# Performance work log

Measured on AMD Instinct MI355X. Metric: run time of the kernel, lower is better.

## Reference

```python
import jax, jax.numpy as jnp
import numpy as np

WIN, SHIFT, HEADS = 12, 6, 24

def _rel_index(win):
    coords = np.stack(np.meshgrid(np.arange(win), np.arange(win), indexing='ij'))  # [2,w,w]
    flat = coords.reshape(2, -1)
    rel = (flat[:, :, None] - flat[:, None, :]).transpose(1, 2, 0).astype(np.int64)  # [N,N,2]
    rel[..., 0] += win - 1
    rel[..., 1] += win - 1
    rel[..., 0] *= 2 * win - 1
    return rel.sum(-1).reshape(-1).astype(np.int32)  # [N*N]

def _shift_mask(H, W, win, shift, dtype):
    img = np.zeros((H, W), np.float32)
    cnt = 0
    for hs in (slice(0, -win), slice(-win, -shift), slice(-shift, None)):
        for ws in (slice(0, -win), slice(-win, -shift), slice(-shift, None)):
            img[hs, ws] = cnt
            cnt += 1
    mw = img.reshape(H // win, win, W // win, win).transpose(0, 2, 1, 3).reshape(-1, win * win)  # [nW,N]
    diff = mw[:, None, :] - mw[:, :, None]
    return jnp.asarray(np.where(diff != 0, -100.0, 0.0), dtype=dtype)  # [nW,N,N]

def setup_inputs() -> dict:
    key = jax.random.key(0)
    ks = jax.random.split(key, 5)
    B, H, W, C = 64, 24, 24, 768
    x = jax.random.normal(ks[0], (B, H, W, C), jnp.float32)
    qkv_w = jax.random.normal(ks[1], (C, 3 * C), jnp.float32) * 0.02
    qkv_b = jnp.zeros((3 * C,), jnp.float32)
    proj_w = jax.random.normal(ks[2], (C, C), jnp.float32) * 0.02
    proj_b = jnp.zeros((C,), jnp.float32)
    rpb_table = jax.random.normal(ks[3], ((2 * WIN - 1) ** 2, HEADS), jnp.float32) * 0.02
    rel_index = jnp.asarray(_rel_index(WIN))
    return {"x": x, "qkv_w": qkv_w, "qkv_b": qkv_b, "proj_w": proj_w,
            "proj_b": proj_b, "rpb_table": rpb_table, "rel_index": rel_index}

def reference(x, qkv_w, qkv_b, proj_w, proj_b, rpb_table, rel_index):
    B, H, W, C = x.shape
    win, shift, heads = WIN, SHIFT, HEADS
    d = C // heads
    scale = d ** -0.5
    N = win * win
    nWh, nWw = H // win, W // win
    nW = nWh * nWw
    # cyclic shift
    xs = jnp.roll(x, (-shift, -shift), axis=(1, 2))
    # window partition -> [B*nW, N, C]
    xw = xs.reshape(B, nWh, win, nWw, win, C).transpose(0, 1, 3, 2, 4, 5).reshape(B * nW, N, C)
    qkv = (xw @ qkv_w + qkv_b).reshape(B * nW, N, 3, heads, d).transpose(2, 0, 3, 1, 4)
    q, k, v = qkv[0] * scale, qkv[1], qkv[2]  # [B*nW, h, N, d]
    attn = jnp.einsum('bhnd,bhmd->bhnm', q, k)
    bias = rpb_table[rel_index].reshape(N, N, heads).transpose(2, 0, 1)  # [h,N,N]
    attn = attn + bias[None]
    mask = _shift_mask(H, W, win, shift, attn.dtype)  # [nW,N,N], static
    attn = (attn.reshape(B, nW, heads, N, N) + mask[None, :, None]).reshape(B * nW, heads, N, N)
    attn = jax.nn.softmax(attn, axis=-1)
    out = jnp.einsum('bhnm,bhmd->bhnd', attn, v).transpose(0, 2, 1, 3).reshape(B * nW, N, C)
    out = out @ proj_w + proj_b
    # window merge + reverse shift
    out = out.reshape(B, nWh, nWw, win, win, C).transpose(0, 1, 3, 2, 4, 5).reshape(B, H, W, C)
    out = jnp.roll(out, (shift, shift), axis=(1, 2))
    # L2 normalize over channel dim (L2N)
    return out / jnp.sqrt(jnp.sum(out * out, axis=-1, keepdims=True) + 1e-6)
```

## Files before the change

kernel.cpp:

```cpp
#include <hip/hip_runtime.h>

typedef unsigned short u16;
typedef __bf16 bf16x8 __attribute__((ext_vector_type(8)));
typedef float f32x4 __attribute__((ext_vector_type(4)));
typedef u16 u16x8 __attribute__((ext_vector_type(8)));
typedef u16 u16x4 __attribute__((ext_vector_type(4)));

__device__ __forceinline__ u16 f2bf(float f) {
    union { float f; unsigned u; } v; v.f = f;
    unsigned r = v.u + 0x7FFFu + ((v.u >> 16) & 1u);
    return (u16)(r >> 16);
}
__device__ __forceinline__ float bf2f(u16 u) {
    union { unsigned u; float f; } v; v.u = ((unsigned)u) << 16; return v.f;
}

#define AS1 __attribute__((address_space(1)))
#define AS3 __attribute__((address_space(3)))
__device__ __forceinline__ void gload_lds16(const void* g, void* l) {
    __builtin_amdgcn_global_load_lds((const AS1 void*)(g), (AS3 void*)(l), 16, 0, 0);
}


__global__ __launch_bounds__(256) void prep_x_kernel(const float* __restrict__ x, u16* __restrict__ xw) {
    unsigned i = ((unsigned)blockIdx.x * 256u + threadIdx.x) * 4u;
    int R = (int)(i / 768u); int c = (int)(i % 768u);
    int w = R / 144, nn = R - w * 144;
    int b = w >> 2, wi = w & 3;
    int r = nn / 12, cc = nn - r * 12;
    int sh = (wi >> 1) * 12 + r + 6; if (sh >= 24) sh -= 24;
    int sw = (wi & 1) * 12 + cc + 6; if (sw >= 24) sw -= 24;
    const float* src = x + (((size_t)b * 24 + sh) * 24 + sw) * 768 + c;
    f32x4 v = *(const f32x4*)src;
    u16x4 o; o[0] = f2bf(v[0]); o[1] = f2bf(v[1]); o[2] = f2bf(v[2]); o[3] = f2bf(v[3]);
    size_t idx = ((size_t)(R >> 7) * 24 + (c >> 5)) * 4096 + (R & 127) * 32 + (c & 31);
    *(u16x4*)(xw + idx) = o;
}

__global__ __launch_bounds__(256) void transpose_cast_kernel(const float* __restrict__ w, u16* __restrict__ wt,
                                                             int K, int N) {
    __shared__ float tile[32][33];
    int tx = threadIdx.x & 31, ty = threadIdx.x >> 5;
    int nb = blockIdx.x * 32, kb = blockIdx.y * 32;
#pragma unroll
    for (int rr = 0; rr < 32; rr += 8) tile[rr + ty][tx] = w[(size_t)(kb + rr + ty) * N + nb + tx];
    __syncthreads();
#pragma unroll
    for (int rr = 0; rr < 32; rr += 8) {
        int n = nb + rr + ty, k = kb + tx;
        wt[((size_t)(n >> 7) * 24 + (k >> 5)) * 4096 + (n & 127) * 32 + (k & 31)] = f2bf(tile[tx][rr + ty]);
    }
}

__global__ __launch_bounds__(256) void make_bias_kernel(const float* __restrict__ tab, const int* __restrict__ rel,
                                                        u16* __restrict__ bm) {
    int i = blockIdx.x * 256 + threadIdx.x;
    int h = i / 20736, nm = i - h * 20736;
    bm[i] = f2bf(tab[rel[nm] * 24 + h]);
}

#define FENCE asm volatile("" ::: "memory")
#define BARRIER __builtin_amdgcn_s_barrier()

#define STAGE_TILE(gp, ldsoff)                                                                 \
    { const char* srcb = (const char*)(gp);                                                    \
      _Pragma("unroll") for (int j = 0; j < 2; j++) {                                          \
        int off = j * 4096 + t * 16;                                                           \
        gload_lds16(srcb + off, (char*)lds + (ldsoff) + off);                                  \
    } }

template <int EPI>
__global__ __launch_bounds__(256, 3) void gemm128_kernel(const u16* __restrict__ A, const u16* __restrict__ Bt,
                                                         const float* __restrict__ bias,
                                                         u16* __restrict__ o0, u16* __restrict__ o1, u16* __restrict__ o2,
                                                         int Ndim, int Kdim, int nxb, int ntiles, float qscale) {
    __shared__ __align__(16) u16 lds[24576];
    const int t = threadIdx.x, lane = t & 63, wv = t >> 6;
    const int wr = wv >> 1, wc = wv & 1;
    const int l15 = lane & 15, lg = lane >> 4;
    const int NT = Kdim >> 5;
    const int q8 = ntiles >> 3, r8 = ntiles & 7;

    int tid = blockIdx.x;
    int xcd = tid & 7, loc = tid >> 3;
    int wg = (xcd < r8 ? xcd * (q8 + 1) : r8 * (q8 + 1) + (xcd - r8) * q8) + loc;
    int by = wg / nxb, bx = wg - by * nxb;
    const u16* Ap = A + (size_t)by * NT * 4096;
    const u16* Bp = Bt + (size_t)bx * NT * 4096;

    STAGE_TILE(Ap, 0);
    STAGE_TILE(Bp, 8192);
    STAGE_TILE(Ap + 4096, 16384);
    STAGE_TILE(Bp + 4096, 16384 + 8192);
    asm volatile("s_waitcnt vmcnt(4)" ::: "memory");
    FENCE; BARRIER;

    while (true) {
        f32x4 acc[4][4] = {};
        int ntid = tid + (int)gridDim.x;
        bool hasNext = ntid < ntiles;
        int nby = 0, nbx = 0;
        const u16 *Anp = nullptr, *Bnp = nullptr;
        if (hasNext) {
            int nxcd = ntid & 7, nloc = ntid >> 3;
            int nwg = (nxcd < r8 ? nxcd * (q8 + 1) : r8 * (q8 + 1) + (nxcd - r8) * q8) + nloc;
            nby = nwg / nxb; nbx = nwg - nby * nxb;
            Anp = A + (size_t)nby * NT * 4096;
            Bnp = Bt + (size_t)nbx * NT * 4096;
        }
        for (int T = 0; T < NT; ++T) {
            const char* rb = (const char*)lds + (T % 3) * 16384;
            const int sb = ((T + 2) % 3) * 16384;
            bool st = true;
            if (T + 2 < NT) {
                STAGE_TILE(Ap + (T + 2) * 4096, sb);
                STAGE_TILE(Bp + (T + 2) * 4096, sb + 8192);
            } else if (hasNext) {
                int TT = T + 2 - NT;
                STAGE_TILE(Anp + TT * 4096, sb);
                STAGE_TILE(Bnp + TT * 4096, sb + 8192);
            } else st = false;
            bf16x8 aR[4], bR[4];
#pragma unroll
            for (int mf = 0; mf < 4; mf++)
                aR[mf] = *(const bf16x8*)(rb + (wr * 64 + mf * 16 + l15) * 64 + lg * 16);
#pragma unroll
            for (int nf = 0; nf < 4; nf++)
                bR[nf] = *(const bf16x8*)(rb + 8192 + (wc * 64 + nf * 16 + l15) * 64 + lg * 16);
            __builtin_amdgcn_s_setprio(1);
#pragma unroll
            for (int mf = 0; mf < 4; mf++)
#pragma unroll
                for (int nf = 0; nf < 4; nf++)
                    acc[mf][nf] = __builtin_amdgcn_mfma_f32_16x16x32_bf16(aR[mf], bR[nf], acc[mf][nf], 0, 0, 0);
            __builtin_amdgcn_s_setprio(0);
            if (T < NT - 1 || hasNext) {
                if (st) { asm volatile("s_waitcnt vmcnt(4)" ::: "memory"); }
                else    { asm volatile("s_waitcnt vmcnt(0)" ::: "memory"); }
                FENCE; BARRIER;
            }
        }
        const int bm = by << 7, bn = bx << 7;
#pragma unroll
        for (int mf = 0; mf < 4; mf++) {
            int Rbase = bm + wr * 64 + mf * 16 + lg * 4;
#pragma unroll
            for (int nf = 0; nf < 4; nf++) {
                int Cg = bn + wc * 64 + nf * 16 + l15;
                float bv = bias[Cg];
                if (EPI == 0) {
                    int s = Cg / 768; int rem = Cg - s * 768; int h = rem >> 5; int dd = rem & 31;
#pragma unroll
                    for (int rg = 0; rg < 4; rg++) {
                        int R = Rbase + rg;
                        int w2 = R / 144; int nn = R - w2 * 144;
                        float v = acc[mf][nf][rg] + bv;
                        if (s == 0)      o0[((size_t)(w2 * 24 + h) * 144 + nn) * 32 + dd] = f2bf(v * qscale);
                        else if (s == 1) o1[((size_t)(w2 * 24 + h) * 144 + nn) * 32 + dd] = f2bf(v);
                        else             o2[((size_t)(w2 * 24 + h) * 32 + dd) * 144 + nn] = f2bf(v);
                    }
                } else {
#pragma unroll
                    for (int rg = 0; rg < 4; rg++) {
                        int R = Rbase + rg;
                        o0[(size_t)R * Ndim + Cg] = f2bf(acc[mf][nf][rg] + bv);
                    }
                }
            }
        }
        if (!hasNext) break;
        tid = ntid; by = nby; bx = nbx; Ap = Anp; Bp = Bnp;
    }
}

__global__ __launch_bounds__(576) void attn_kernel(const u16* __restrict__ Qg, const u16* __restrict__ Kg,
                                                   const u16* __restrict__ Vg, const u16* __restrict__ bias_mat,
                                                   u16* __restrict__ Ob) {
    __shared__ __align__(16) u16 Qs[144 * 40];
    __shared__ __align__(16) u16 Ks[144 * 40];
    __shared__ __align__(16) u16 Vs[32 * 160];
    __shared__ __align__(16) u16 Ps[144 * 160];
    const int bx = blockIdx.x;
    const int w = bx / 24, h = bx - w * 24;
    const int wi = w & 3, wh = wi >> 1, ww = wi & 1;
    const int t = threadIdx.x, lane = t & 63, wv = t >> 6;
    const int l15 = lane & 15, lg = lane >> 4;
    const size_t base = (size_t)bx * 4608;
    {
        int nn = t >> 2, dd = (t & 3) << 3;
        *(u16x8*)(Qs + nn * 40 + dd) = *(const u16x8*)(Qg + base + nn * 32 + dd);
        *(u16x8*)(Ks + nn * 40 + dd) = *(const u16x8*)(Kg + base + nn * 32 + dd);
        int rv = t / 18, cv = (t - rv * 18) * 8;
        int ba = (rv * 320 + cv * 2) ^ ((rv & 7) << 4);
        *(u16x8*)((char*)Vs + ba) = *(const u16x8*)(Vg + base + rv * 144 + cv);
    }
    u16x8 zz = (u16x8)0;
    if (t < 64)  { int rv = t >> 1, cv = 144 + (t & 1) * 8; int ba = (rv * 320 + cv * 2) ^ ((rv & 7) << 4); *(u16x8*)((char*)Vs + ba) = zz; }
    if (t < 288) { int rv = t >> 1, cv = 144 + (t & 1) * 8; int ba = (rv * 320 + cv * 2) ^ ((rv & 7) << 4); *(u16x8*)((char*)Ps + ba) = zz; }
    __syncthreads();

    f32x4 S[9];
    {
        bf16x8 aq = *(const bf16x8*)(Qs + (wv * 16 + l15) * 40 + lg * 8);
        f32x4 z4 = (f32x4)0.0f;
#pragma unroll
        for (int j = 0; j < 9; j++) {
            bf16x8 bk = *(const bf16x8*)(Ks + (j * 16 + l15) * 40 + lg * 8);
            S[j] = __builtin_amdgcn_mfma_f32_16x16x32_bf16(aq, bk, z4, 0, 0, 0);
        }
    }
    int regm[9];
#pragma unroll
    for (int j = 0; j < 9; j++) {
        int m = j * 16 + l15; int r = m / 12, c = m - r * 12;
        int rid = wh ? (r < 6 ? 1 : 2) : 0;
        int cid = ww ? (c < 6 ? 1 : 2) : 0;
        regm[j] = rid * 3 + cid;
    }
    const u16* bh = bias_mat + h * 20736;
#pragma unroll
    for (int rg = 0; rg < 4; rg++) {
        int n = wv * 16 + lg * 4 + rg;
        int r = n / 12, c = n - r * 12;
        int rid = wh ? (r < 6 ? 1 : 2) : 0;
        int cid = ww ? (c < 6 ? 1 : 2) : 0;
        int regn = rid * 3 + cid;
        const u16* bhn = bh + n * 144;
        float mx = -1e30f;
#pragma unroll
        for (int j = 0; j < 9; j++) {
            float v = S[j][rg] + bf2f(bhn[j * 16 + l15]);
            if (regn != regm[j]) v -= 100.0f;
            S[j][rg] = v;
            mx = fmaxf(mx, v);
        }
#pragma unroll
        for (int d = 1; d < 16; d <<= 1) mx = fmaxf(mx, __shfl_xor(mx, d));
        float sum = 0.0f;
#pragma unroll
        for (int j = 0; j < 9; j++) { float e = __expf(S[j][rg] - mx); S[j][rg] = e; sum += e; }
#pragma unroll
        for (int d = 1; d < 16; d <<= 1) sum += __shfl_xor(sum, d);
        float inv = 1.0f / sum;
#pragma unroll
        for (int j = 0; j < 9; j++) {
            int ba = (n * 320 + (j * 16 + l15) * 2) ^ ((n & 7) << 4);
            *(u16*)((char*)Ps + ba) = f2bf(S[j][rg] * inv);
        }
    }
    __syncthreads();
    f32x4 o0 = (f32x4)0.0f, o1 = (f32x4)0.0f;
#pragma unroll
    for (int ks = 0; ks < 5; ks++) {
        int k2 = (ks * 32 + lg * 8) * 2;
        int ra = wv * 16 + l15;
        bf16x8 ap = *(const bf16x8*)((char*)Ps + ((ra * 320 + k2) ^ ((ra & 7) << 4)));
        int rv0 = l15, rv1 = 16 + l15;
        bf16x8 b0 = *(const bf16x8*)((char*)Vs + ((rv0 * 320 + k2) ^ ((rv0 & 7) << 4)));
        bf16x8 b1 = *(const bf16x8*)((char*)Vs + ((rv1 * 320 + k2) ^ ((rv1 & 7) << 4)));
        o0 = __builtin_amdgcn_mfma_f32_16x16x32_bf16(ap, b0, o0, 0, 0, 0);
        o1 = __builtin_amdgcn_mfma_f32_16x16x32_bf16(ap, b1, o1, 0, 0, 0);
    }
#pragma unroll
    for (int rg = 0; rg < 4; rg++) {
        int n = wv * 16 + lg * 4 + rg;
        int R = w * 144 + n;
        size_t idx = ((size_t)(R >> 7) * 24 + h) * 4096 + (R & 127) * 32;
        Ob[idx + l15]      = f2bf(o0[rg]);
        Ob[idx + 16 + l15] = f2bf(o1[rg]);
    }
}

__global__ __launch_bounds__(256) void norm_kernel(const u16* __restrict__ raw, float* __restrict__ out) {
    int R = blockIdx.x * 4 + (threadIdx.x >> 6);
    int lane = threadIdx.x & 63;
    const u16* src = raw + (size_t)R * 768;
    u16x8 a = *(const u16x8*)(src + lane * 8);
    u16x4 b = *(const u16x4*)(src + 512 + lane * 4);
    float f[12];
#pragma unroll
    for (int k = 0; k < 8; k++) f[k] = bf2f(a[k]);
#pragma unroll
    for (int k = 0; k < 4; k++) f[8 + k] = bf2f(b[k]);
    float ss = 0.0f;
#pragma unroll
    for (int k = 0; k < 12; k++) ss += f[k] * f[k];
#pragma unroll
    for (int d = 1; d < 64; d <<= 1) ss += __shfl_xor(ss, d);
    float inv = 1.0f / sqrtf(ss + 1e-6f);
    int w = R / 144, nn = R - w * 144;
    int bb = w >> 2, wi = w & 3;
    int r = nn / 12, cc = nn - r * 12;
    int oh = (wi >> 1) * 12 + r + 6; if (oh >= 24) oh -= 24;
    int ow = (wi & 1) * 12 + cc + 6; if (ow >= 24) ow -= 24;
    float* dst = out + (((size_t)bb * 24 + oh) * 24 + ow) * 768;
    f32x4 v0, v1, v2;
#pragma unroll
    for (int k = 0; k < 4; k++) { v0[k] = f[k] * inv; v1[k] = f[4 + k] * inv; v2[k] = f[8 + k] * inv; }
    *(f32x4*)(dst + lane * 8) = v0;
    *(f32x4*)(dst + lane * 8 + 4) = v1;
    *(f32x4*)(dst + 512 + lane * 4) = v2;
}

extern "C" void kernel_launch(void* const* d_in, const int* in_sizes, int n_in,
                              void* d_out, int out_size, void* d_ws, size_t ws_size,
                              hipStream_t stream) {
    const float* x      = (const float*)d_in[0];
    const float* qkv_w  = (const float*)d_in[1];
    const float* qkv_b  = (const float*)d_in[2];
    const float* proj_w = (const float*)d_in[3];
    const float* proj_b = (const float*)d_in[4];
    const float* rpb    = (const float*)d_in[5];
    const int*   rel    = (const int*)d_in[6];

    char* ws = (char*)d_ws;
    const size_t SZ = 56623104;
    u16*   xw   = (u16*)(ws);
    u16*   Qb   = (u16*)(ws + SZ);
    u16*   Kb   = (u16*)(ws + 2 * SZ);
    u16*   Vt   = (u16*)(ws + 3 * SZ);
    u16*   Ob   = (u16*)(ws + 4 * SZ);
    u16*   qwt  = (u16*)(ws + 5 * SZ);
    u16*   pwt  = (u16*)(ws + 5 * SZ + 3538944);
    u16*   bm   = (u16*)(ws + 5 * SZ + 3538944 + 1179648);
    u16*   raw16 = (u16*)(ws);

    prep_x_kernel<<<27648, 256, 0, stream>>>(x, xw);
    transpose_cast_kernel<<<dim3(72, 24), 256, 0, stream>>>(qkv_w, qwt, 768, 2304);
    transpose_cast_kernel<<<dim3(24, 24), 256, 0, stream>>>(proj_w, pwt, 768, 768);
    make_bias_kernel<<<1944, 256, 0, stream>>>(rpb, rel, bm);

    gemm128_kernel<0><<<768, 256, 0, stream>>>(xw, qwt, qkv_b, Qb, Kb, Vt,
                                               2304, 768, 18, 5184, 0.17677669529663687f);
    attn_kernel<<<6144, 576, 0, stream>>>(Qb, Kb, Vt, bm, Ob);
    gemm128_kernel<1><<<768, 256, 0, stream>>>(Ob, pwt, proj_b, raw16, nullptr, nullptr,
                                               768, 768, 6, 1728, 1.0f);
    norm_kernel<<<9216, 256, 0, stream>>>(raw16, (float*)d_out);
}
```

Before: 460.3 us.

## Keep softmax probabilities in registers and compute transposed S in attention kernel

```diff
diff --git a/kernel.cpp b/kernel.cpp
--- a/kernel.cpp
+++ b/kernel.cpp
@@ -5,6 +5,7 @@
 typedef float f32x4 __attribute__((ext_vector_type(4)));
 typedef u16 u16x8 __attribute__((ext_vector_type(8)));
 typedef u16 u16x4 __attribute__((ext_vector_type(4)));
+typedef unsigned u32x4 __attribute__((ext_vector_type(4)));
 
 __device__ __forceinline__ u16 f2bf(float f) {
     union { float f; unsigned u; } v; v.f = f;
@@ -13,6 +14,11 @@
 }
 __device__ __forceinline__ float bf2f(u16 u) {
     union { unsigned u; float f; } v; v.u = ((unsigned)u) << 16; return v.f;
+}
+__device__ __forceinline__ unsigned cvt_pk_bf16(float lo, float hi) {
+    unsigned r;
+    asm("v_cvt_pk_bf16_f32 %0, %1, %2" : "=v"(r) : "v"(lo), "v"(hi));
+    return r;
 }
 
 #define AS1 __attribute__((address_space(1)))
@@ -55,8 +61,9 @@
 __global__ __launch_bounds__(256) void make_bias_kernel(const float* __restrict__ tab, const int* __restrict__ rel,
                                                         u16* __restrict__ bm) {
     int i = blockIdx.x * 256 + threadIdx.x;
-    int h = i / 20736, nm = i - h * 20736;
-    bm[i] = f2bf(tab[rel[nm] * 24 + h]);
+    int h = i / 20736, mn = i - h * 20736;
+    int m = mn / 144, n = mn - m * 144;
+    bm[i] = f2bf(tab[rel[n * 144 + m] * 24 + h]);
 }
 
 #define FENCE asm volatile("" ::: "memory")
@@ -173,101 +180,117 @@
     }
 }
 
-__global__ __launch_bounds__(576) void attn_kernel(const u16* __restrict__ Qg, const u16* __restrict__ Kg,
-                                                   const u16* __restrict__ Vg, const u16* __restrict__ bias_mat,
+__global__ __launch_bounds__(192) void attn_kernel(const u16* __restrict__ Qg, const u16* __restrict__ Kg,
+                                                   const u16* __restrict__ Vg, const u16* __restrict__ bmT,
                                                    u16* __restrict__ Ob) {
-    __shared__ __align__(16) u16 Qs[144 * 40];
     __shared__ __align__(16) u16 Ks[144 * 40];
     __shared__ __align__(16) u16 Vs[32 * 160];
-    __shared__ __align__(16) u16 Ps[144 * 160];
     const int bx = blockIdx.x;
     const int w = bx / 24, h = bx - w * 24;
     const int wi = w & 3, wh = wi >> 1, ww = wi & 1;
     const int t = threadIdx.x, lane = t & 63, wv = t >> 6;
     const int l15 = lane & 15, lg = lane >> 4;
     const size_t base = (size_t)bx * 4608;
-    {
-        int nn = t >> 2, dd = (t & 3) << 3;
-        *(u16x8*)(Qs + nn * 40 + dd) = *(const u16x8*)(Qg + base + nn * 32 + dd);
-        *(u16x8*)(Ks + nn * 40 + dd) = *(const u16x8*)(Kg + base + nn * 32 + dd);
-        int rv = t / 18, cv = (t - rv * 18) * 8;
+#pragma unroll
+    for (int p = 0; p < 3; p++) {
+        int e = t + p * 192;
+        int row = e >> 2, cx = (e & 3) << 3;
+        *(u16x8*)(Ks + row * 40 + cx) = *(const u16x8*)(Kg + base + row * 32 + cx);
+        int rv = e / 18, cv = (e - rv * 18) * 8;
         int ba = (rv * 320 + cv * 2) ^ ((rv & 7) << 4);
         *(u16x8*)((char*)Vs + ba) = *(const u16x8*)(Vg + base + rv * 144 + cv);
     }
-    u16x8 zz = (u16x8)0;
-    if (t < 64)  { int rv = t >> 1, cv = 144 + (t & 1) * 8; int ba = (rv * 320 + cv * 2) ^ ((rv & 7) << 4); *(u16x8*)((char*)Vs + ba) = zz; }
-    if (t < 288) { int rv = t >> 1, cv = 144 + (t & 1) * 8; int ba = (rv * 320 + cv * 2) ^ ((rv & 7) << 4); *(u16x8*)((char*)Ps + ba) = zz; }
+    if (t < 64) {
+        u16x8 zz = (u16x8)0;
+        int rv = t >> 1, cv = 144 + (t & 1) * 8;
+        int ba = (rv * 320 + cv * 2) ^ ((rv & 7) << 4);
+        *(u16x8*)((char*)Vs + ba) = zz;
+    }
     __syncthreads();
 
-    f32x4 S[9];
-    {
-        bf16x8 aq = *(const bf16x8*)(Qs + (wv * 16 + l15) * 40 + lg * 8);
-        f32x4 z4 = (f32x4)0.0f;
+    const u16* bh = bmT + h * 20736;
+#pragma unroll 1
+    for (int it = 0; it < 3; ++it) {
+        const int s = wv * 3 + it;
+        const int q = s * 16 + l15;
+        bf16x8 aq = *(const bf16x8*)(Qg + base + (size_t)q * 32 + lg * 8);
+        f32x4 S[9];
+        {
+            f32x4 z4 = (f32x4)0.0f;
+#pragma unroll
+            for (int j = 0; j < 9; j++) {
+                bf16x8 bk = *(const bf16x8*)(Ks + (j * 16 + l15) * 40 + lg * 8);
+                S[j] = __builtin_amdgcn_mfma_f32_16x16x32_bf16(bk, aq, z4, 0, 0, 0);
+            }
+        }
+        int rq = q / 12, cq = q - rq * 12; int r12 = rq - s * 0;
+        int ridn = wh ? ((rq % 12) < 6 ? 1 : 2) : 0;
+        int cidn = ww ? (cq < 6 ? 1 : 2) : 0;
+        int regn = ridn * 3 + cidn;
+        (void)r12;
+        float mx = -1e30f;
 #pragma unroll
         for (int j = 0; j < 9; j++) {
-            bf16x8 bk = *(const bf16x8*)(Ks + (j * 16 + l15) * 40 + lg * 8);
-            S[j] = __builtin_amdgcn_mfma_f32_16x16x32_bf16(aq, bk, z4, 0, 0, 0);
-        }
-    }
-    int regm[9];
-#pragma unroll
-    for (int j = 0; j < 9; j++) {
-        int m = j * 16 + l15; int r = m / 12, c = m - r * 12;
-        int rid = wh ? (r < 6 ? 1 : 2) : 0;
-        int cid = ww ? (c < 6 ? 1 : 2) : 0;
-        regm[j] = rid * 3 + cid;
-    }
-    const u16* bh = bias_mat + h * 20736;
-#pragma unroll
-    for (int rg = 0; rg < 4; rg++) {
-        int n = wv * 16 + lg * 4 + rg;
-        int r = n / 12, c = n - r * 12;
-        int rid = wh ? (r < 6 ? 1 : 2) : 0;
-        int cid = ww ? (c < 6 ? 1 : 2) : 0;
-        int regn = rid * 3 + cid;
-        const u16* bhn = bh + n * 144;
-        float mx = -1e30f;
+            const u16* bj = bh + (j * 16 + lg * 4) * 144 + q;
+#pragma unroll
+            for (int rg = 0; rg < 4; rg++) {
+                int k = j * 16 + lg * 4 + rg;
+                int rk = k / 12, ck = k - rk * 12;
+                int ridm = wh ? (rk < 6 ? 1 : 2) : 0;
+                int cidm = ww ? (ck < 6 ? 1 : 2) : 0;
+                float v = S[j][rg] + bf2f(bj[rg * 144]);
+                if (regn != (ridm * 3 + cidm)) v -= 100.0f;
+                S[j][rg] = v;
+                mx = fmaxf(mx, v);
+            }
+        }
+        mx = fmaxf(mx, __shfl_xor(mx, 16));
+        mx = fmaxf(mx, __shfl_xor(mx, 32));
+        float sum = 0.0f;
 #pragma unroll
         for (int j = 0; j < 9; j++) {
-            float v = S[j][rg] + bf2f(bhn[j * 16 + l15]);
-            if (regn != regm[j]) v -= 100.0f;
-            S[j][rg] = v;
-            mx = fmaxf(mx, v);
-        }
-#pragma unroll
-        for (int d = 1; d < 16; d <<= 1) mx = fmaxf(mx, __shfl_xor(mx, d));
-        float sum = 0.0f;
-#pragma unroll
-        for (int j = 0; j < 9; j++) { float e = __expf(S[j][rg] - mx); S[j][rg] = e; sum += e; }
-#pragma unroll
-        for (int d = 1; d < 16; d <<= 1) sum += __shfl_xor(sum, d);
+#pragma unroll
+            for (int rg = 0; rg < 4; rg++) { float e = __expf(S[j][rg] - mx); S[j][rg] = e; sum += e; }
+        }
+        sum += __shfl_xor(sum, 16);
+        sum += __shfl_xor(sum, 32);
         float inv = 1.0f / sum;
+        unsigned pk[10][2];
 #pragma unroll
         for (int j = 0; j < 9; j++) {
-            int ba = (n * 320 + (j * 16 + l15) * 2) ^ ((n & 7) << 4);
-            *(u16*)((char*)Ps + ba) = f2bf(S[j][rg] * inv);
-        }
-    }
-    __syncthreads();
-    f32x4 o0 = (f32x4)0.0f, o1 = (f32x4)0.0f;
-#pragma unroll
-    for (int ks = 0; ks < 5; ks++) {
-        int k2 = (ks * 32 + lg * 8) * 2;
-        int ra = wv * 16 + l15;
-        bf16x8 ap = *(const bf16x8*)((char*)Ps + ((ra * 320 + k2) ^ ((ra & 7) << 4)));
-        int rv0 = l15, rv1 = 16 + l15;
-        bf16x8 b0 = *(const bf16x8*)((char*)Vs + ((rv0 * 320 + k2) ^ ((rv0 & 7) << 4)));
-        bf16x8 b1 = *(const bf16x8*)((char*)Vs + ((rv1 * 320 + k2) ^ ((rv1 & 7) << 4)));
-        o0 = __builtin_amdgcn_mfma_f32_16x16x32_bf16(ap, b0, o0, 0, 0, 0);
-        o1 = __builtin_amdgcn_mfma_f32_16x16x32_bf16(ap, b1, o1, 0, 0, 0);
-    }
-#pragma unroll
-    for (int rg = 0; rg < 4; rg++) {
-        int n = wv * 16 + lg * 4 + rg;
-        int R = w * 144 + n;
-        size_t idx = ((size_t)(R >> 7) * 24 + h) * 4096 + (R & 127) * 32;
-        Ob[idx + l15]      = f2bf(o0[rg]);
-        Ob[idx + 16 + l15] = f2bf(o1[rg]);
+            pk[j][0] = cvt_pk_bf16(S[j][0], S[j][1]);
+            pk[j][1] = cvt_pk_bf16(S[j][2], S[j][3]);
+        }
+        pk[9][0] = 0; pk[9][1] = 0;
+        f32x4 o0 = (f32x4)0.0f, o1 = (f32x4)0.0f;
+        const int srcA = 32 * (lg & 1) + l15;
+        const int srcB = srcA + 16;
+        const bool lowj = (lg < 2);
+#pragma unroll
+        for (int ks = 0; ks < 5; ks++) {
+            const int j0 = 2 * ks, j1 = 2 * ks + 1;
+            unsigned a0 = __shfl(pk[j0][0], srcA), a1 = __shfl(pk[j0][1], srcA);
+            unsigned a2 = __shfl(pk[j0][0], srcB), a3 = __shfl(pk[j0][1], srcB);
+            unsigned b0 = __shfl(pk[j1][0], srcA), b1 = __shfl(pk[j1][1], srcA);
+            unsigned b2 = __shfl(pk[j1][0], srcB), b3 = __shfl(pk[j1][1], srcB);
+            u32x4 pw;
+            pw[0] = lowj ? a0 : b0; pw[1] = lowj ? a1 : b1;
+            pw[2] = lowj ? a2 : b2; pw[3] = lowj ? a3 : b3;
+            bf16x8 pb = *(const bf16x8*)&pw;
+            int k2 = (ks * 32 + lg * 8) * 2;
+            int rv0 = l15, rv1 = 16 + l15;
+            bf16x8 v0 = *(const bf16x8*)((char*)Vs + ((rv0 * 320 + k2) ^ ((rv0 & 7) << 4)));
+            bf16x8 v1 = *(const bf16x8*)((char*)Vs + ((rv1 * 320 + k2) ^ ((rv1 & 7) << 4)));
+            o0 = __builtin_amdgcn_mfma_f32_16x16x32_bf16(v0, pb, o0, 0, 0, 0);
+            o1 = __builtin_amdgcn_mfma_f32_16x16x32_bf16(v1, pb, o1, 0, 0, 0);
+        }
+        int R = w * 144 + q;
+        size_t idx = ((size_t)(R >> 7) * 24 + h) * 4096 + (R & 127) * 32 + lg * 4;
+        u16x4 w0, w1;
+#pragma unroll
+        for (int rg = 0; rg < 4; rg++) { w0[rg] = f2bf(o0[rg] * inv); w1[rg] = f2bf(o1[rg] * inv); }
+        *(u16x4*)(Ob + idx) = w0;
+        *(u16x4*)(Ob + idx + 16) = w1;
     }
 }
 
@@ -332,7 +355,7 @@
 
     gemm128_kernel<0><<<768, 256, 0, stream>>>(xw, qwt, qkv_b, Qb, Kb, Vt,
                                                2304, 768, 18, 5184, 0.17677669529663687f);
-    attn_kernel<<<6144, 576, 0, stream>>>(Qb, Kb, Vt, bm, Ob);
+    attn_kernel<<<6144, 192, 0, stream>>>(Qb, Kb, Vt, bm, Ob);
     gemm128_kernel<1><<<768, 256, 0, stream>>>(Ob, pwt, proj_b, raw16, nullptr, nullptr,
                                                768, 768, 6, 1728, 1.0f);
     norm_kernel<<<9216, 256, 0, stream>>>(raw16, (float*)d_out);
```

New measurement: 425.6 us. -7.5%, faster.
